# Kernel tuning notes

Hardware: AMD Instinct MI355X
Metric: run time of the kernel (lower is better)

## Reference

```python
import jax, jax.numpy as jnp
import numpy as np

NUM_HEADS = 8
KEY_DIM = 256
EPS = 1e-16


def setup_inputs() -> dict:
    key = jax.random.key(0)
    k1, k2, k3, k4 = jax.random.split(key, 4)
    b, n, d, m = 2, 20000, 256, 320000
    q = jax.random.normal(k1, (b, n, d), dtype=jnp.float32)
    k = jax.random.normal(k2, (b, n, d), dtype=jnp.float32)
    e = jax.random.randint(k3, (2, m), 0, n, dtype=jnp.int64)
    r = jax.random.randint(k4, (m,), 0, n, dtype=jnp.int64)
    return {"q": q, "k": k, "e": e, "r": r}


def reference(q, k, e, r):
    b, n, d = q.shape
    m = e.shape[1]
    dh = d // NUM_HEADS
    # gather edge endpoints, multiply, sum within each head's d_head chunk
    # (scatter_sum over dim with h=[i//dh] == reshape + sum over last axis)
    src_q = q[:, e[0], :]                      # (b, m, d)
    dst_k = k[:, e[1], :]                      # (b, m, d)
    a = (src_q * dst_k).reshape(b, m, NUM_HEADS, dh).sum(-1)  # (b, m, H)
    a = a / jnp.sqrt(jnp.asarray(KEY_DIM, a.dtype))
    # segment softmax over edges grouped by r (global max subtraction, as in source)
    a = a - a.max()
    ex = jnp.exp(a)                            # (b, m, H)
    seg = jax.ops.segment_sum(ex.transpose(1, 0, 2), r, num_segments=n)  # (n, b, H)
    denom = seg[r].transpose(1, 0, 2)          # (b, m, H)
    return ex / (denom + EPS)
```

## Files before the change

kernel.cpp:

```cpp
#include <hip/hip_runtime.h>
#include <hip/hip_bf16.h>
#include <cmath>

#define D 256
#define NH 8
#define B 2
#define EPW 4

__device__ inline unsigned short f2bf(float f) {
    unsigned u = __float_as_uint(f);
    unsigned r = u + 0x7FFFu + ((u >> 16) & 1u);
    return (unsigned short)(r >> 16);
}

__global__ __launch_bounds__(256) void k_conv(
    const float* __restrict__ q, const float* __restrict__ k,
    ushort4* __restrict__ qc, ushort4* __restrict__ kc, int n)
{
    int total = n * B * (D / 4);
    for (int i = blockIdx.x * blockDim.x + threadIdx.x; i < total;
         i += gridDim.x * blockDim.x) {
        int d4  = i & 63;
        int row = i >> 6;
        int bb  = (row >= n) ? 1 : 0;
        int node = row - bb * n;
        const float4 a = ((const float4*)q)[(size_t)row * 64 + d4];
        const float4 b = ((const float4*)k)[(size_t)row * 64 + d4];
        size_t dst = ((size_t)node * B + bb) * 64 + d4;
        qc[dst] = make_ushort4(f2bf(a.x), f2bf(a.y), f2bf(a.z), f2bf(a.w));
        kc[dst] = make_ushort4(f2bf(b.x), f2bf(b.y), f2bf(b.z), f2bf(b.w));
    }
}

__global__ __launch_bounds__(256) void k_scores_fused(
    const ushort* __restrict__ qc, const ushort* __restrict__ kc,
    const int* __restrict__ e, const int* __restrict__ r,
    float* __restrict__ s, float* __restrict__ seg, int m)
{
    int wave = (int)((blockIdx.x * blockDim.x + threadIdx.x) >> 6);
    int lane = threadIdx.x & 63;
    int j0 = wave * EPW;
    if (j0 >= m) return;

    int e0[EPW], e1[EPW], rr[EPW];
    #pragma unroll
    for (int t = 0; t < EPW; ++t) {
        int j = j0 + t;
        int ok = (j < m);
        e0[t] = ok ? e[j]     : 0;
        e1[t] = ok ? e[m + j] : 0;
        rr[t] = ok ? r[j]     : 0;
    }
    uint4 qa[EPW], kb[EPW];
    #pragma unroll
    for (int t = 0; t < EPW; ++t) {
        qa[t] = ((const uint4*)(qc + (size_t)e0[t] * (B * D)))[lane];
        kb[t] = ((const uint4*)(kc + (size_t)e1[t] * (B * D)))[lane];
    }
    #pragma unroll
    for (int t = 0; t < EPW; ++t) {
        float p = 0.f;
        const unsigned* qw = (const unsigned*)&qa[t];
        const unsigned* kw = (const unsigned*)&kb[t];
        #pragma unroll
        for (int w = 0; w < 4; ++w) {
            float ql = __uint_as_float(qw[w] << 16);
            float qh = __uint_as_float(qw[w] & 0xFFFF0000u);
            float kl = __uint_as_float(kw[w] << 16);
            float kh = __uint_as_float(kw[w] & 0xFFFF0000u);
            p = fmaf(ql, kl, p);
            p = fmaf(qh, kh, p);
        }
        p += __shfl_xor(p, 1);
        p += __shfl_xor(p, 2);
        float ex = expf(p * 0.0625f);
        if ((lane & 3) == 0 && (j0 + t) < m) {
            int bb = lane >> 5;
            int h  = (lane >> 2) & 7;
            s[((size_t)bb * m + (j0 + t)) * NH + h] = ex;
            atomicAdd(&seg[((size_t)rr[t] * B + bb) * NH + h], ex);
        }
    }
}

__global__ __launch_bounds__(256) void k_scores_fused_f32(
    const float* __restrict__ q, const float* __restrict__ k,
    const int* __restrict__ e, const int* __restrict__ r,
    float* __restrict__ s, float* __restrict__ seg, int n, int m)
{
    int wave = (int)((blockIdx.x * blockDim.x + threadIdx.x) >> 6);
    int lane = threadIdx.x & 63;
    int j0 = wave * EPW;
    if (j0 >= m) return;
    int e0[EPW], e1[EPW], rr[EPW];
    #pragma unroll
    for (int t = 0; t < EPW; ++t) {
        int j = j0 + t; int ok = (j < m);
        e0[t] = ok ? e[j] : 0; e1[t] = ok ? e[m + j] : 0; rr[t] = ok ? r[j] : 0;
    }
    float4 qa[B][EPW], kb[B][EPW];
    #pragma unroll
    for (int bb = 0; bb < B; ++bb)
        #pragma unroll
        for (int t = 0; t < EPW; ++t) {
            qa[bb][t] = ((const float4*)(q + ((size_t)bb * n + e0[t]) * D))[lane];
            kb[bb][t] = ((const float4*)(k + ((size_t)bb * n + e1[t]) * D))[lane];
        }
    #pragma unroll
    for (int bb = 0; bb < B; ++bb)
        #pragma unroll
        for (int t = 0; t < EPW; ++t) {
            float4 A = qa[bb][t], K4 = kb[bb][t];
            float p = A.x * K4.x + A.y * K4.y + A.z * K4.z + A.w * K4.w;
            p += __shfl_xor(p, 1); p += __shfl_xor(p, 2); p += __shfl_xor(p, 4);
            float ex = expf(p * 0.0625f);
            if ((lane & 7) == 0 && (j0 + t) < m) {
                int h = lane >> 3;
                s[((size_t)bb * m + (j0 + t)) * NH + h] = ex;
                atomicAdd(&seg[((size_t)rr[t] * B + bb) * NH + h], ex);
            }
        }
}

__global__ __launch_bounds__(256) void k_norm(
    float* __restrict__ s, const int* __restrict__ r,
    const float* __restrict__ seg, int m)
{
    int i = blockIdx.x * blockDim.x + threadIdx.x;
    int total = B * m;
    if (i >= total) return;
    int bb = (i >= m) ? 1 : 0;
    int j  = i - bb * m;
    const float4* sg = (const float4*)(seg + ((size_t)r[j] * B + bb) * NH);
    float4* sp = (float4*)(s + (size_t)i * NH);
    float4 d0 = sg[0], d1 = sg[1];
    float4 x0 = sp[0], x1 = sp[1];
    x0.x /= (d0.x + 1e-16f); x0.y /= (d0.y + 1e-16f);
    x0.z /= (d0.z + 1e-16f); x0.w /= (d0.w + 1e-16f);
    x1.x /= (d1.x + 1e-16f); x1.y /= (d1.y + 1e-16f);
    x1.z /= (d1.z + 1e-16f); x1.w /= (d1.w + 1e-16f);
    sp[0] = x0; sp[1] = x1;
}

extern "C" void kernel_launch(void* const* d_in, const int* in_sizes, int n_in,
                              void* d_out, int out_size, void* d_ws, size_t ws_size,
                              hipStream_t stream) {
    const float* q = (const float*)d_in[0];
    const float* k = (const float*)d_in[1];
    const int*   e = (const int*)d_in[2];
    const int*   r = (const int*)d_in[3];
    float* s = (float*)d_out;

    int n = in_sizes[0] / (B * D);
    int m = in_sizes[3];
    int nwaves = (m + EPW - 1) / EPW;

    size_t seg_bytes = (size_t)n * B * NH * sizeof(float);
    size_t row_bytes = (size_t)n * B * D * sizeof(unsigned short);
    float*  seg = (float*)d_ws;
    ushort* qc  = (ushort*)((char*)d_ws + seg_bytes);
    ushort* kc  = (ushort*)((char*)d_ws + seg_bytes + row_bytes);
    bool use_bf16 = ws_size >= (seg_bytes + 2 * row_bytes);

    hipMemsetAsync(d_ws, 0, seg_bytes, stream);

    int sblocks = (nwaves + 3) / 4;
    int nblocks = (B * m + 255) / 256;

    if (use_bf16) {
        k_conv<<<4096, 256, 0, stream>>>(q, k, (ushort4*)qc, (ushort4*)kc, n);
        k_scores_fused<<<sblocks, 256, 0, stream>>>(qc, kc, e, r, s, seg, m);
    } else {
        k_scores_fused_f32<<<sblocks, 256, 0, stream>>>(q, k, e, r, s, seg, n, m);
    }
    k_norm<<<nblocks, 256, 0, stream>>>(s, r, seg, m);
}
```

Measured before the change: 215.4 us.

## Widen bf16 conversion stores, double edges per wave, use fast exp/div

The conversion kernel now has each thread handle 8 floats and write one 16-byte packed bf16 store, and its grid is sized to the data instead of a fixed grid-stride launch. The bf16 scores kernel processes 8 edges per wave instead of 4 and interleaves index loads with row gathers, with a sched_barrier to keep all loads issued ahead of the math. This gives more memory-level parallelism at the cost of more registers. expf and the division in normalization are replaced with the fast intrinsics, which are slightly less accurate.

```diff
diff --git a/kernel.cpp b/kernel.cpp
--- a/kernel.cpp
+++ b/kernel.cpp
@@ -5,7 +5,8 @@
 #define D 256
 #define NH 8
 #define B 2
-#define EPW 4
+#define EPW 8
+#define EPW32 4
 
 __device__ inline unsigned short f2bf(float f) {
     unsigned u = __float_as_uint(f);
@@ -15,20 +16,31 @@
 
 __global__ __launch_bounds__(256) void k_conv(
     const float* __restrict__ q, const float* __restrict__ k,
-    ushort4* __restrict__ qc, ushort4* __restrict__ kc, int n)
+    uint4* __restrict__ qc, uint4* __restrict__ kc, int n)
 {
-    int total = n * B * (D / 4);
+    int total = n * B * 32;
     for (int i = blockIdx.x * blockDim.x + threadIdx.x; i < total;
          i += gridDim.x * blockDim.x) {
-        int d4  = i & 63;
-        int row = i >> 6;
+        int c   = i & 31;
+        int row = i >> 5;
         int bb  = (row >= n) ? 1 : 0;
         int node = row - bb * n;
-        const float4 a = ((const float4*)q)[(size_t)row * 64 + d4];
-        const float4 b = ((const float4*)k)[(size_t)row * 64 + d4];
-        size_t dst = ((size_t)node * B + bb) * 64 + d4;
-        qc[dst] = make_ushort4(f2bf(a.x), f2bf(a.y), f2bf(a.z), f2bf(a.w));
-        kc[dst] = make_ushort4(f2bf(b.x), f2bf(b.y), f2bf(b.z), f2bf(b.w));
+        const float4* qs = (const float4*)(q + ((size_t)row << 8)) + (c << 1);
+        const float4* ks = (const float4*)(k + ((size_t)row << 8)) + (c << 1);
+        float4 a0 = qs[0], a1 = qs[1];
+        float4 b0 = ks[0], b1 = ks[1];
+        uint4 pa, pb;
+        pa.x = (unsigned)f2bf(a0.x) | ((unsigned)f2bf(a0.y) << 16);
+        pa.y = (unsigned)f2bf(a0.z) | ((unsigned)f2bf(a0.w) << 16);
+        pa.z = (unsigned)f2bf(a1.x) | ((unsigned)f2bf(a1.y) << 16);
+        pa.w = (unsigned)f2bf(a1.z) | ((unsigned)f2bf(a1.w) << 16);
+        pb.x = (unsigned)f2bf(b0.x) | ((unsigned)f2bf(b0.y) << 16);
+        pb.y = (unsigned)f2bf(b0.z) | ((unsigned)f2bf(b0.w) << 16);
+        pb.z = (unsigned)f2bf(b1.x) | ((unsigned)f2bf(b1.y) << 16);
+        pb.w = (unsigned)f2bf(b1.z) | ((unsigned)f2bf(b1.w) << 16);
+        size_t dst = ((size_t)node * B + bb) * 32 + c;
+        qc[dst] = pa;
+        kc[dst] = pb;
     }
 }
 
@@ -42,21 +54,20 @@
     int j0 = wave * EPW;
     if (j0 >= m) return;
 
-    int e0[EPW], e1[EPW], rr[EPW];
+    int rr[EPW];
+    uint4 qa[EPW], kb[EPW];
     #pragma unroll
     for (int t = 0; t < EPW; ++t) {
         int j = j0 + t;
         int ok = (j < m);
-        e0[t] = ok ? e[j]     : 0;
-        e1[t] = ok ? e[m + j] : 0;
-        rr[t] = ok ? r[j]     : 0;
+        int e0 = ok ? e[j]     : 0;
+        int e1 = ok ? e[m + j] : 0;
+        rr[t] = ok ? r[j]      : 0;
+        qa[t] = ((const uint4*)(qc + (size_t)e0 * (B * D)))[lane];
+        kb[t] = ((const uint4*)(kc + (size_t)e1 * (B * D)))[lane];
     }
-    uint4 qa[EPW], kb[EPW];
-    #pragma unroll
-    for (int t = 0; t < EPW; ++t) {
-        qa[t] = ((const uint4*)(qc + (size_t)e0[t] * (B * D)))[lane];
-        kb[t] = ((const uint4*)(kc + (size_t)e1[t] * (B * D)))[lane];
-    }
+    __builtin_amdgcn_sched_barrier(0);
+
     #pragma unroll
     for (int t = 0; t < EPW; ++t) {
         float p = 0.f;
@@ -73,7 +84,7 @@
         }
         p += __shfl_xor(p, 1);
         p += __shfl_xor(p, 2);
-        float ex = expf(p * 0.0625f);
+        float ex = __expf(p * 0.0625f);
         if ((lane & 3) == 0 && (j0 + t) < m) {
             int bb = lane >> 5;
             int h  = (lane >> 2) & 7;
@@ -90,30 +101,31 @@
 {
     int wave = (int)((blockIdx.x * blockDim.x + threadIdx.x) >> 6);
     int lane = threadIdx.x & 63;
-    int j0 = wave * EPW;
+    int j0 = wave * EPW32;
     if (j0 >= m) return;
-    int e0[EPW], e1[EPW], rr[EPW];
+    int e0[EPW32], e1[EPW32], rr[EPW32];
     #pragma unroll
-    for (int t = 0; t < EPW; ++t) {
+    for (int t = 0; t < EPW32; ++t) {
         int j = j0 + t; int ok = (j < m);
         e0[t] = ok ? e[j] : 0; e1[t] = ok ? e[m + j] : 0; rr[t] = ok ? r[j] : 0;
     }
-    float4 qa[B][EPW], kb[B][EPW];
+    float4 qa[B][EPW32], kb[B][EPW32];
     #pragma unroll
     for (int bb = 0; bb < B; ++bb)
         #pragma unroll
-        for (int t = 0; t < EPW; ++t) {
+        for (int t = 0; t < EPW32; ++t) {
             qa[bb][t] = ((const float4*)(q + ((size_t)bb * n + e0[t]) * D))[lane];
             kb[bb][t] = ((const float4*)(k + ((size_t)bb * n + e1[t]) * D))[lane];
         }
+    __builtin_amdgcn_sched_barrier(0);
     #pragma unroll
     for (int bb = 0; bb < B; ++bb)
         #pragma unroll
-        for (int t = 0; t < EPW; ++t) {
+        for (int t = 0; t < EPW32; ++t) {
             float4 A = qa[bb][t], K4 = kb[bb][t];
             float p = A.x * K4.x + A.y * K4.y + A.z * K4.z + A.w * K4.w;
             p += __shfl_xor(p, 1); p += __shfl_xor(p, 2); p += __shfl_xor(p, 4);
-            float ex = expf(p * 0.0625f);
+            float ex = __expf(p * 0.0625f);
             if ((lane & 7) == 0 && (j0 + t) < m) {
                 int h = lane >> 3;
                 s[((size_t)bb * m + (j0 + t)) * NH + h] = ex;
@@ -135,10 +147,14 @@
     float4* sp = (float4*)(s + (size_t)i * NH);
     float4 d0 = sg[0], d1 = sg[1];
     float4 x0 = sp[0], x1 = sp[1];
-    x0.x /= (d0.x + 1e-16f); x0.y /= (d0.y + 1e-16f);
-    x0.z /= (d0.z + 1e-16f); x0.w /= (d0.w + 1e-16f);
-    x1.x /= (d1.x + 1e-16f); x1.y /= (d1.y + 1e-16f);
-    x1.z /= (d1.z + 1e-16f); x1.w /= (d1.w + 1e-16f);
+    x0.x = __fdividef(x0.x, d0.x + 1e-16f);
+    x0.y = __fdividef(x0.y, d0.y + 1e-16f);
+    x0.z = __fdividef(x0.z, d0.z + 1e-16f);
+    x0.w = __fdividef(x0.w, d0.w + 1e-16f);
+    x1.x = __fdividef(x1.x, d1.x + 1e-16f);
+    x1.y = __fdividef(x1.y, d1.y + 1e-16f);
+    x1.z = __fdividef(x1.z, d1.z + 1e-16f);
+    x1.w = __fdividef(x1.w, d1.w + 1e-16f);
     sp[0] = x0; sp[1] = x1;
 }
 
@@ -153,7 +169,6 @@
 
     int n = in_sizes[0] / (B * D);
     int m = in_sizes[3];
-    int nwaves = (m + EPW - 1) / EPW;
 
     size_t seg_bytes = (size_t)n * B * NH * sizeof(float);
     size_t row_bytes = (size_t)n * B * D * sizeof(unsigned short);
@@ -164,13 +179,17 @@
 
     hipMemsetAsync(d_ws, 0, seg_bytes, stream);
 
-    int sblocks = (nwaves + 3) / 4;
     int nblocks = (B * m + 255) / 256;
 
     if (use_bf16) {
-        k_conv<<<4096, 256, 0, stream>>>(q, k, (ushort4*)qc, (ushort4*)kc, n);
+        int cblocks = (n * B * 32 + 255) / 256;
+        int nwaves  = (m + EPW - 1) / EPW;
+        int sblocks = (nwaves + 3) / 4;
+        k_conv<<<cblocks, 256, 0, stream>>>(q, k, (uint4*)qc, (uint4*)kc, n);
         k_scores_fused<<<sblocks, 256, 0, stream>>>(qc, kc, e, r, s, seg, m);
     } else {
+        int nwaves  = (m + EPW32 - 1) / EPW32;
+        int sblocks = (nwaves + 3) / 4;
         k_scores_fused_f32<<<sblocks, 256, 0, stream>>>(q, k, e, r, s, seg, n, m);
     }
     k_norm<<<nblocks, 256, 0, stream>>>(s, r, seg, m);
```

Result: slower. 226.5 us (+5.2%).
